# Optimization experiments

Hardware: AMD Instinct MI355X
Metric: run time of the kernel (lower is better)

Reference implementation:

```python
import jax, jax.numpy as jnp
import numpy as np

B, T, C = 4, 2048, 1024
H = 16
DH = C // H  # 64


def setup_inputs() -> dict:
    key = jax.random.key(0)
    ks = jax.random.split(key, 6)
    s = 1.0 / np.sqrt(C)
    x = jax.random.normal(ks[0], (B, T, C), dtype=jnp.float32)
    # per-head projection weights, stacked: (H, C, DH)
    Wq = jax.random.uniform(ks[1], (H, C, DH), dtype=jnp.float32, minval=-s, maxval=s)
    Wk = jax.random.uniform(ks[2], (H, C, DH), dtype=jnp.float32, minval=-s, maxval=s)
    Wv = jax.random.uniform(ks[3], (H, C, DH), dtype=jnp.float32, minval=-s, maxval=s)
    # output projection (torch Linear: y = x @ W.T + b); store as (C, C) for x @ Wo
    Wo = jax.random.uniform(ks[4], (C, C), dtype=jnp.float32, minval=-s, maxval=s)
    bo = jax.random.uniform(ks[5], (C,), dtype=jnp.float32, minval=-s, maxval=s)
    return {"x": x, "Wq": Wq, "Wk": Wk, "Wv": Wv, "Wo": Wo, "bo": bo}


def reference(x, Wq, Wk, Wv, Wo, bo):
    # x: (B,T,C) -> q,k,v: (B,H,T,DH)
    q = jnp.einsum('btc,hcd->bhtd', x, Wq)
    k = jnp.einsum('btc,hcd->bhtd', x, Wk)
    v = jnp.einsum('btc,hcd->bhtd', x, Wv)
    scale = DH ** -0.5
    scores = jnp.einsum('bhtd,bhsd->bhts', q, k) * scale  # (B,H,T,T)
    causal = jnp.tril(jnp.ones((T, T), dtype=bool))
    scores = jnp.where(causal, scores, -jnp.inf)
    wei = jax.nn.softmax(scores, axis=-1)
    out = jnp.einsum('bhts,bhsd->bhtd', wei, v)  # (B,H,T,DH)
    # concat heads: (B,T,H*DH) = (B,T,C)
    out = out.transpose(0, 2, 1, 3).reshape(B, T, C)
    return out @ Wo + bo
```

## Files before the change

kernel.cpp:

```cpp
#include <hip/hip_runtime.h>

#define T_SEQ 2048
#define C_DIM 1024
#define H_NUM 16
#define DHD   64
#define B_NUM 4
#define M_ROWS (B_NUM*T_SEQ)

typedef __bf16 bf16x8 __attribute__((ext_vector_type(8)));
typedef float  f32x4  __attribute__((ext_vector_type(4)));
typedef unsigned short ushort8 __attribute__((ext_vector_type(8)));
typedef unsigned short ushort4e __attribute__((ext_vector_type(4)));

__device__ __forceinline__ unsigned short f2b(float f){
  return __builtin_bit_cast(unsigned short, (__bf16)f);
}
__device__ __forceinline__ bf16x8 as_bf(ushort8 u){ return __builtin_bit_cast(bf16x8, u); }
__device__ __forceinline__ float exp2fast(float x){ return __builtin_amdgcn_exp2f(x); }

__device__ __forceinline__ void gload16(const void* g, void* l){
  __builtin_amdgcn_global_load_lds(
      (const __attribute__((address_space(1))) void*)g,
      (__attribute__((address_space(3))) void*)l, 16, 0, 0);
}

__global__ __launch_bounds__(256) void k_conv_x(const float* __restrict__ x,
                                                unsigned short* __restrict__ xb){
  int i = blockIdx.x*256 + threadIdx.x;
  float4 f = ((const float4*)x)[i];
  ushort4e o;
  o[0]=f2b(f.x); o[1]=f2b(f.y); o[2]=f2b(f.z); o[3]=f2b(f.w);
  ((ushort4e*)xb)[i] = o;
}

__global__ __launch_bounds__(256) void k_pack_w(const float* __restrict__ wq,
                                                const float* __restrict__ wk,
                                                const float* __restrict__ wv,
                                                const float* __restrict__ wo,
                                                unsigned short* __restrict__ wt,
                                                unsigned short* __restrict__ wot){
  int idx = blockIdx.x*256 + threadIdx.x;
  if (idx < 3*C_DIM*C_DIM){
    int nall = idx >> 10; int c = idx & 1023;
    int m = nall >> 10;   int n = nall & 1023;
    int h = n >> 6, d = n & 63;
    const float* w = (m==0) ? wq : (m==1) ? wk : wv;
    float f = w[((size_t)h*C_DIM + c)*DHD + d];
    if (m == 0) f *= 0.125f * 1.4426950408889634f;
    wt[idx] = f2b(f);
  } else {
    int j = idx - 3*C_DIM*C_DIM;
    int n = j >> 10, c = j & 1023;
    wot[j] = f2b(wo[(size_t)c*C_DIM + n]);
  }
}

__global__ __launch_bounds__(256) void k_gemm_qkv(const unsigned short* __restrict__ xb,
                                                  const unsigned short* __restrict__ wt,
                                                  unsigned short* __restrict__ qo,
                                                  unsigned short* __restrict__ ko,
                                                  unsigned short* __restrict__ vtr){
  __shared__ __align__(16) unsigned short smem[2][128*64];
  const int tid = threadIdx.x, lane = tid & 63, wid = tid >> 6;
  const int g = lane >> 4, tl = lane & 15;
  const int wr = wid >> 1, wc = wid & 1;
  const int id = blockIdx.x;
  const int swz = (id & 7)*192 + (id >> 3);
  const int mbase = (swz / 24) * 128, nbase = (swz % 24) * 128;
  f32x4 acc[4][4] = {};
  for (int kk = 0; kk < C_DIM; kk += 64){
    __syncthreads();
    #pragma unroll
    for (int i = 0; i < 4; i++){
      const int brow = (wid*4 + i)*8;
      const int row  = brow + (lane >> 3);
      const int jj   = (lane & 7) ^ (row & 7);
      gload16(&xb[(size_t)(mbase+row)*C_DIM + kk + jj*8], &smem[0][brow*64]);
      gload16(&wt[(size_t)(nbase+row)*C_DIM + kk + jj*8], &smem[1][brow*64]);
    }
    __syncthreads();
    bf16x8 aF[4][2], bF[4][2];
    #pragma unroll
    for (int mb = 0; mb < 4; mb++){
      const int row = wr*64 + mb*16 + tl; const int s7 = row & 7;
      aF[mb][0] = as_bf(*(const ushort8*)&smem[0][row*64 + ((g     ^ s7)*8)]);
      aF[mb][1] = as_bf(*(const ushort8*)&smem[0][row*64 + (((4+g) ^ s7)*8)]);
    }
    #pragma unroll
    for (int nb = 0; nb < 4; nb++){
      const int row = wc*64 + nb*16 + tl; const int s7 = row & 7;
      bF[nb][0] = as_bf(*(const ushort8*)&smem[1][row*64 + ((g     ^ s7)*8)]);
      bF[nb][1] = as_bf(*(const ushort8*)&smem[1][row*64 + (((4+g) ^ s7)*8)]);
    }
    #pragma unroll
    for (int mb = 0; mb < 4; mb++)
      #pragma unroll
      for (int nb = 0; nb < 4; nb++){
        acc[mb][nb] = __builtin_amdgcn_mfma_f32_16x16x32_bf16(aF[mb][0], bF[nb][0], acc[mb][nb], 0,0,0);
        acc[mb][nb] = __builtin_amdgcn_mfma_f32_16x16x32_bf16(aF[mb][1], bF[nb][1], acc[mb][nb], 0,0,0);
      }
  }
  const int sel = nbase >> 10;
  if (sel < 2){
    unsigned short* dst0 = (sel == 0) ? qo : ko;
    #pragma unroll
    for (int mb = 0; mb < 4; mb++){
      #pragma unroll
      for (int nb = 0; nb < 4; nb++){
        #pragma unroll
        for (int r = 0; r < 4; r++){
          int gr = mbase + wr*64 + mb*16 + g*4 + r;
          int gc = nbase + wc*64 + nb*16 + tl;
          int b = gr >> 11, t = gr & 2047;
          int nw = gc & 1023;
          int h = nw >> 6, d = nw & 63;
          dst0[(((size_t)(b*H_NUM + h))*T_SEQ + t)*DHD + d] = f2b(acc[mb][nb][r]);
        }
      }
    }
  } else {
    __syncthreads();
    unsigned short* tr = &smem[0][0];
    #pragma unroll
    for (int mb = 0; mb < 4; mb++){
      #pragma unroll
      for (int nb = 0; nb < 4; nb++){
        const int n = wc*64 + nb*16 + tl;
        const int m0 = wr*64 + mb*16 + g*4;
        ushort4e pk;
        #pragma unroll
        for (int r = 0; r < 4; r++) pk[r] = f2b(acc[mb][nb][r]);
        *(ushort4e*)&tr[n*128 + (m0 ^ ((n & 15) << 3))] = pk;
      }
    }
    __syncthreads();
    const int hbase = (nbase - 2048) >> 6;
    const int b = mbase >> 11, tloc = mbase & 2047;
    const int n = tid >> 1, half = tid & 1;
    unsigned short* vdst = vtr + (((size_t)(b*H_NUM + hbase + (n >> 6)))*DHD + (n & 63))*T_SEQ
                           + tloc + half*64;
    #pragma unroll
    for (int c8 = 0; c8 < 8; c8++){
      const int chunk = (half*8 + c8) ^ (n & 15);
      *(ushort8*)&vdst[c8*8] = *(const ushort8*)&tr[n*128 + chunk*8];
    }
  }
}

__global__ __launch_bounds__(512) void k_flash(const unsigned short* __restrict__ q,
                                               const unsigned short* __restrict__ k,
                                               const unsigned short* __restrict__ vtg,
                                               unsigned short* __restrict__ o){
  __shared__ __align__(16) unsigned short kbufs[2][64*64];
  __shared__ __align__(16) unsigned short vbufs[2][64*64];
  __shared__ __align__(16) unsigned short pl[8][32][72];
  const int tid = threadIdx.x, lane = tid & 63, w = tid >> 6;
  const int g = lane >> 4, tl = lane & 15;
  const int id = blockIdx.x;
  const int swz = (id & 7)*32 + (id >> 3);
  const int bh = swz >> 2, bx = swz & 3;
  const int b = bh >> 4, h = bh & 15;
  const unsigned short* qb = q   + (size_t)bh * T_SEQ * DHD;
  const unsigned short* kb = k   + (size_t)bh * T_SEQ * DHD;
  const unsigned short* vb = vtg + (size_t)bh * (size_t)DHD * T_SEQ;
  const int lrow = lane >> 3, lj = lane & 7;

  for (int pass = 0; pass < 2; ++pass){
    const int qt = pass ? (7 - bx) : bx;
    const int tbase = qt * 256;
    const int trow0 = tbase + w * 32;
    const int tmax = trow0 + 31;
    bf16x8 qF[2][2];
    #pragma unroll
    for (int tf = 0; tf < 2; tf++)
      #pragma unroll
      for (int ks = 0; ks < 2; ks++)
        qF[tf][ks] = as_bf(*(const ushort8*)&qb[(size_t)(trow0 + tf*16 + tl)*DHD + ks*32 + g*8]);
    f32x4 acc[2][4] = {};
    float mreg[2] = {-1e30f, -1e30f}, lreg[2] = {0.f, 0.f};
    const int nkt = 4*qt + 4;
    {
      const int row = w*8 + lrow;
      const int jj = lj ^ (row & 7);
      gload16(&kb[(size_t)row*DHD + jj*8],   &kbufs[0][w*8*64]);
      gload16(&vb[(size_t)row*T_SEQ + jj*8], &vbufs[0][w*8*64]);
    }
    __syncthreads();
    for (int kti = 0; kti < nkt; ++kti){
      const int cur = kti & 1;
      const int kbase = kti * 64;
      if (kti + 1 < nkt){
        const int kb2 = kbase + 64;
        const int row = w*8 + lrow;
        const int jj = lj ^ (row & 7);
        gload16(&kb[(size_t)(kb2+row)*DHD + jj*8],   &kbufs[cur^1][w*8*64]);
        gload16(&vb[(size_t)row*T_SEQ + kb2 + jj*8], &vbufs[cur^1][w*8*64]);
      }
      if (kbase <= tmax){
        const unsigned short* kcur = kbufs[cur];
        const unsigned short* vcur = vbufs[cur];
        const int s7 = tl & 7;
        f32x4 st[2][4] = {};
        __builtin_amdgcn_s_setprio(1);
        #pragma unroll
        for (int sf = 0; sf < 4; sf++){
          const int row = sf*16 + tl;
          bf16x8 kf0 = as_bf(*(const ushort8*)&kcur[row*64 + ((g     ^ s7)*8)]);
          bf16x8 kf1 = as_bf(*(const ushort8*)&kcur[row*64 + (((4+g) ^ s7)*8)]);
          #pragma unroll
          for (int tf = 0; tf < 2; tf++){
            st[tf][sf] = __builtin_amdgcn_mfma_f32_16x16x32_bf16(kf0, qF[tf][0], st[tf][sf], 0,0,0);
            st[tf][sf] = __builtin_amdgcn_mfma_f32_16x16x32_bf16(kf1, qF[tf][1], st[tf][sf], 0,0,0);
          }
        }
        __builtin_amdgcn_s_setprio(0);
        if (kbase + 63 > trow0){
          #pragma unroll
          for (int tf = 0; tf < 2; tf++){
            int tg = trow0 + tf*16 + tl;
            #pragma unroll
            for (int sf = 0; sf < 4; sf++)
              #pragma unroll
              for (int r = 0; r < 4; r++)
                if (kbase + sf*16 + g*4 + r > tg) st[tf][sf][r] = -1e30f;
          }
        }
        #pragma unroll
        for (int tf = 0; tf < 2; tf++){
          float mloc = -1e30f;
          #pragma unroll
          for (int sf = 0; sf < 4; sf++)
            #pragma unroll
            for (int r = 0; r < 4; r++) mloc = fmaxf(mloc, st[tf][sf][r]);
          if (__any(mloc > mreg[tf] + 8.f)){
            float mrow = fmaxf(mloc, __shfl_xor(mloc, 16));
            mrow = fmaxf(mrow, __shfl_xor(mrow, 32));
            float mnew = fmaxf(mreg[tf], mrow);
            float alpha = exp2fast(mreg[tf] - mnew);
            mreg[tf] = mnew;
            lreg[tf] *= alpha;
            #pragma unroll
            for (int df = 0; df < 4; df++)
              #pragma unroll
              for (int r = 0; r < 4; r++) acc[tf][df][r] *= alpha;
          }
          float sum = 0.f;
          #pragma unroll
          for (int sf = 0; sf < 4; sf++){
            ushort4e pk;
            #pragma unroll
            for (int r = 0; r < 4; r++){
              float p = exp2fast(st[tf][sf][r] - mreg[tf]);
              sum += p;
              pk[r] = f2b(p);
            }
            *(ushort4e*)&pl[w][tf*16 + tl][sf*16 + g*4] = pk;
          }
          lreg[tf] += sum;
        }
        bf16x8 pa[2][2];
        #pragma unroll
        for (int tf = 0; tf < 2; tf++)
          #pragma unroll
          for (int ks = 0; ks < 2; ks++)
            pa[tf][ks] = as_bf(*(const ushort8*)&pl[w][tf*16 + tl][ks*32 + g*8]);
        __builtin_amdgcn_s_setprio(1);
        #pragma unroll
        for (int df = 0; df < 4; df++){
          const int row = df*16 + tl;
          bf16x8 vf0 = as_bf(*(const ushort8*)&vcur[row*64 + ((g     ^ s7)*8)]);
          bf16x8 vf1 = as_bf(*(const ushort8*)&vcur[row*64 + (((4+g) ^ s7)*8)]);
          #pragma unroll
          for (int tf = 0; tf < 2; tf++){
            acc[tf][df] = __builtin_amdgcn_mfma_f32_16x16x32_bf16(vf0, pa[tf][0], acc[tf][df], 0,0,0);
            acc[tf][df] = __builtin_amdgcn_mfma_f32_16x16x32_bf16(vf1, pa[tf][1], acc[tf][df], 0,0,0);
          }
        }
        __builtin_amdgcn_s_setprio(0);
      }
      __syncthreads();
    }
    #pragma unroll
    for (int tf = 0; tf < 2; tf++){
      float l = lreg[tf];
      l += __shfl_xor(l, 16);
      l += __shfl_xor(l, 32);
      float inv = 1.f / l;
      int tg = trow0 + tf*16 + tl;
      #pragma unroll
      for (int df = 0; df < 4; df++){
        ushort4e ov;
        #pragma unroll
        for (int r = 0; r < 4; r++) ov[r] = f2b(acc[tf][df][r] * inv);
        *(ushort4e*)&o[((size_t)(b*T_SEQ + tg))*C_DIM + h*DHD + df*16 + g*4] = ov;
      }
    }
  }
}

__global__ __launch_bounds__(256) void k_gemm_proj(const unsigned short* __restrict__ ab,
                                                   const unsigned short* __restrict__ wot,
                                                   const float* __restrict__ bo,
                                                   float* __restrict__ out){
  __shared__ __align__(16) unsigned short a_lds[128*64];
  __shared__ __align__(16) unsigned short b_lds[128*64];
  const int tid = threadIdx.x, lane = tid & 63, wid = tid >> 6;
  const int g = lane >> 4, tl = lane & 15;
  const int wr = wid >> 1, wc = wid & 1;
  const int id = blockIdx.x;
  const int swz = (id & 7)*64 + (id >> 3);
  const int mbase = (swz >> 3) * 128, nbase = (swz & 7) * 128;
  f32x4 acc[4][4] = {};
  for (int kk = 0; kk < C_DIM; kk += 64){
    __syncthreads();
    #pragma unroll
    for (int i = 0; i < 4; i++){
      const int brow = (wid*4 + i)*8;
      const int row  = brow + (lane >> 3);
      const int jj   = (lane & 7) ^ (row & 7);
      gload16(&ab[(size_t)(mbase+row)*C_DIM + kk + jj*8],  &a_lds[brow*64]);
      gload16(&wot[(size_t)(nbase+row)*C_DIM + kk + jj*8], &b_lds[brow*64]);
    }
    __syncthreads();
    bf16x8 aF[4][2], bF[4][2];
    #pragma unroll
    for (int mb = 0; mb < 4; mb++){
      const int row = wr*64 + mb*16 + tl; const int s7 = row & 7;
      aF[mb][0] = as_bf(*(const ushort8*)&a_lds[row*64 + ((g     ^ s7)*8)]);
      aF[mb][1] = as_bf(*(const ushort8*)&a_lds[row*64 + (((4+g) ^ s7)*8)]);
    }
    #pragma unroll
    for (int nb = 0; nb < 4; nb++){
      const int row = wc*64 + nb*16 + tl; const int s7 = row & 7;
      bF[nb][0] = as_bf(*(const ushort8*)&b_lds[row*64 + ((g     ^ s7)*8)]);
      bF[nb][1] = as_bf(*(const ushort8*)&b_lds[row*64 + (((4+g) ^ s7)*8)]);
    }
    #pragma unroll
    for (int mb = 0; mb < 4; mb++)
      #pragma unroll
      for (int nb = 0; nb < 4; nb++){
        acc[mb][nb] = __builtin_amdgcn_mfma_f32_16x16x32_bf16(aF[mb][0], bF[nb][0], acc[mb][nb], 0,0,0);
        acc[mb][nb] = __builtin_amdgcn_mfma_f32_16x16x32_bf16(aF[mb][1], bF[nb][1], acc[mb][nb], 0,0,0);
      }
  }
  #pragma unroll
  for (int mb = 0; mb < 4; mb++){
    #pragma unroll
    for (int nb = 0; nb < 4; nb++){
      #pragma unroll
      for (int r = 0; r < 4; r++){
        int gr = mbase + wr*64 + mb*16 + g*4 + r;
        int gc = nbase + wc*64 + nb*16 + tl;
        out[(size_t)gr*C_DIM + gc] = acc[mb][nb][r] + bo[gc];
      }
    }
  }
}

extern "C" void kernel_launch(void* const* d_in, const int* in_sizes, int n_in,
                              void* d_out, int out_size, void* d_ws, size_t ws_size,
                              hipStream_t stream){
  const float* x  = (const float*)d_in[0];
  const float* Wq = (const float*)d_in[1];
  const float* Wk = (const float*)d_in[2];
  const float* Wv = (const float*)d_in[3];
  const float* Wo = (const float*)d_in[4];
  const float* bo = (const float*)d_in[5];
  float* out = (float*)d_out;

  char* p = (char*)d_ws;
  unsigned short* xb  = (unsigned short*)p; p += (size_t)M_ROWS*C_DIM*2;
  unsigned short* wt  = (unsigned short*)p; p += (size_t)3*C_DIM*C_DIM*2;
  unsigned short* wot = (unsigned short*)p; p += (size_t)C_DIM*C_DIM*2;
  unsigned short* Qb  = (unsigned short*)p; p += (size_t)M_ROWS*C_DIM*2;
  unsigned short* Kb  = (unsigned short*)p; p += (size_t)M_ROWS*C_DIM*2;
  unsigned short* Vtr = (unsigned short*)p; p += (size_t)M_ROWS*C_DIM*2;
  unsigned short* attn = xb;

  hipLaunchKernelGGL(k_conv_x, dim3(M_ROWS*C_DIM/4/256), dim3(256), 0, stream, x, xb);
  hipLaunchKernelGGL(k_pack_w, dim3(4*C_DIM*C_DIM/256), dim3(256), 0, stream,
                     Wq, Wk, Wv, Wo, wt, wot);
  hipLaunchKernelGGL(k_gemm_qkv, dim3(1536), dim3(256), 0, stream,
                     xb, wt, Qb, Kb, Vtr);
  hipLaunchKernelGGL(k_flash, dim3(256), dim3(512), 0, stream,
                     Qb, Kb, Vtr, attn);
  hipLaunchKernelGGL(k_gemm_proj, dim3(512), dim3(256), 0, stream,
                     attn, wot, bo, out);
}
```

Measured before the change: 183.3 us.

## Keep softmax probabilities in registers and merge prep kernels into one launch

The flash kernel no longer writes the exp'd scores to an LDS staging buffer and reads them back. It packs them straight into bf16 MFMA operands in registers, and reorders how V fragments are read from LDS so their k-index layout matches the accumulator layout. This removes the per-wave LDS round trip and the 36KB of shared memory it used, which may also allow higher occupancy. Separately, the x conversion and weight packing kernels are merged into one launch to save a kernel launch. The V loads are now two 8-byte reads per fragment instead of one 16-byte read.

```diff
diff --git a/kernel.cpp b/kernel.cpp
--- a/kernel.cpp
+++ b/kernel.cpp
@@ -24,34 +24,38 @@
       (__attribute__((address_space(3))) void*)l, 16, 0, 0);
 }
 
-__global__ __launch_bounds__(256) void k_conv_x(const float* __restrict__ x,
-                                                unsigned short* __restrict__ xb){
-  int i = blockIdx.x*256 + threadIdx.x;
-  float4 f = ((const float4*)x)[i];
-  ushort4e o;
-  o[0]=f2b(f.x); o[1]=f2b(f.y); o[2]=f2b(f.z); o[3]=f2b(f.w);
-  ((ushort4e*)xb)[i] = o;
-}
-
-__global__ __launch_bounds__(256) void k_pack_w(const float* __restrict__ wq,
-                                                const float* __restrict__ wk,
-                                                const float* __restrict__ wv,
-                                                const float* __restrict__ wo,
-                                                unsigned short* __restrict__ wt,
-                                                unsigned short* __restrict__ wot){
-  int idx = blockIdx.x*256 + threadIdx.x;
-  if (idx < 3*C_DIM*C_DIM){
-    int nall = idx >> 10; int c = idx & 1023;
-    int m = nall >> 10;   int n = nall & 1023;
-    int h = n >> 6, d = n & 63;
-    const float* w = (m==0) ? wq : (m==1) ? wk : wv;
-    float f = w[((size_t)h*C_DIM + c)*DHD + d];
-    if (m == 0) f *= 0.125f * 1.4426950408889634f;
-    wt[idx] = f2b(f);
+#define MF(a,b,c) __builtin_amdgcn_mfma_f32_16x16x32_bf16(a,b,c,0,0,0)
+
+__global__ __launch_bounds__(256) void k_prep(const float* __restrict__ x,
+                                              const float* __restrict__ wq,
+                                              const float* __restrict__ wk,
+                                              const float* __restrict__ wv,
+                                              const float* __restrict__ wo,
+                                              unsigned short* __restrict__ xb,
+                                              unsigned short* __restrict__ wt,
+                                              unsigned short* __restrict__ wot){
+  const int bid = blockIdx.x;
+  if (bid < 8192){
+    int i = bid*256 + threadIdx.x;
+    float4 f = ((const float4*)x)[i];
+    ushort4e o;
+    o[0]=f2b(f.x); o[1]=f2b(f.y); o[2]=f2b(f.z); o[3]=f2b(f.w);
+    ((ushort4e*)xb)[i] = o;
   } else {
-    int j = idx - 3*C_DIM*C_DIM;
-    int n = j >> 10, c = j & 1023;
-    wot[j] = f2b(wo[(size_t)c*C_DIM + n]);
+    int idx = (bid - 8192)*256 + threadIdx.x;
+    if (idx < 3*C_DIM*C_DIM){
+      int nall = idx >> 10; int c = idx & 1023;
+      int m = nall >> 10;   int n = nall & 1023;
+      int h = n >> 6, d = n & 63;
+      const float* w = (m==0) ? wq : (m==1) ? wk : wv;
+      float f = w[((size_t)h*C_DIM + c)*DHD + d];
+      if (m == 0) f *= 0.125f * 1.4426950408889634f;
+      wt[idx] = f2b(f);
+    } else {
+      int j = idx - 3*C_DIM*C_DIM;
+      int n = j >> 10, c = j & 1023;
+      wot[j] = f2b(wo[(size_t)c*C_DIM + n]);
+    }
   }
 }
 
@@ -96,8 +100,8 @@
     for (int mb = 0; mb < 4; mb++)
       #pragma unroll
       for (int nb = 0; nb < 4; nb++){
-        acc[mb][nb] = __builtin_amdgcn_mfma_f32_16x16x32_bf16(aF[mb][0], bF[nb][0], acc[mb][nb], 0,0,0);
-        acc[mb][nb] = __builtin_amdgcn_mfma_f32_16x16x32_bf16(aF[mb][1], bF[nb][1], acc[mb][nb], 0,0,0);
+        acc[mb][nb] = MF(aF[mb][0], bF[nb][0], acc[mb][nb]);
+        acc[mb][nb] = MF(aF[mb][1], bF[nb][1], acc[mb][nb]);
       }
   }
   const int sel = nbase >> 10;
@@ -153,7 +157,6 @@
                                                unsigned short* __restrict__ o){
   __shared__ __align__(16) unsigned short kbufs[2][64*64];
   __shared__ __align__(16) unsigned short vbufs[2][64*64];
-  __shared__ __align__(16) unsigned short pl[8][32][72];
   const int tid = threadIdx.x, lane = tid & 63, w = tid >> 6;
   const int g = lane >> 4, tl = lane & 15;
   const int id = blockIdx.x;
@@ -209,8 +212,8 @@
           bf16x8 kf1 = as_bf(*(const ushort8*)&kcur[row*64 + (((4+g) ^ s7)*8)]);
           #pragma unroll
           for (int tf = 0; tf < 2; tf++){
-            st[tf][sf] = __builtin_amdgcn_mfma_f32_16x16x32_bf16(kf0, qF[tf][0], st[tf][sf], 0,0,0);
-            st[tf][sf] = __builtin_amdgcn_mfma_f32_16x16x32_bf16(kf1, qF[tf][1], st[tf][sf], 0,0,0);
+            st[tf][sf] = MF(kf0, qF[tf][0], st[tf][sf]);
+            st[tf][sf] = MF(kf1, qF[tf][1], st[tf][sf]);
           }
         }
         __builtin_amdgcn_s_setprio(0);
@@ -246,34 +249,46 @@
           }
           float sum = 0.f;
           #pragma unroll
-          for (int sf = 0; sf < 4; sf++){
-            ushort4e pk;
+          for (int sf = 0; sf < 4; sf++)
             #pragma unroll
             for (int r = 0; r < 4; r++){
               float p = exp2fast(st[tf][sf][r] - mreg[tf]);
               sum += p;
-              pk[r] = f2b(p);
+              st[tf][sf][r] = p;
             }
-            *(ushort4e*)&pl[w][tf*16 + tl][sf*16 + g*4] = pk;
-          }
           lreg[tf] += sum;
         }
         bf16x8 pa[2][2];
         #pragma unroll
         for (int tf = 0; tf < 2; tf++)
           #pragma unroll
-          for (int ks = 0; ks < 2; ks++)
-            pa[tf][ks] = as_bf(*(const ushort8*)&pl[w][tf*16 + tl][ks*32 + g*8]);
+          for (int ks = 0; ks < 2; ks++){
+            ushort8 u;
+            #pragma unroll
+            for (int r = 0; r < 4; r++){
+              u[r]   = f2b(st[tf][2*ks  ][r]);
+              u[4+r] = f2b(st[tf][2*ks+1][r]);
+            }
+            pa[tf][ks] = as_bf(u);
+          }
         __builtin_amdgcn_s_setprio(1);
         #pragma unroll
         for (int df = 0; df < 4; df++){
           const int row = df*16 + tl;
-          bf16x8 vf0 = as_bf(*(const ushort8*)&vcur[row*64 + ((g     ^ s7)*8)]);
-          bf16x8 vf1 = as_bf(*(const ushort8*)&vcur[row*64 + (((4+g) ^ s7)*8)]);
+          bf16x8 vfr[2];
+          #pragma unroll
+          for (int ks = 0; ks < 2; ks++){
+            ushort4e lo = *(const ushort4e*)&vcur[row*64 + (((4*ks +     (g>>1)) ^ s7)*8) + 4*(g&1)];
+            ushort4e hi = *(const ushort4e*)&vcur[row*64 + (((4*ks + 2 + (g>>1)) ^ s7)*8) + 4*(g&1)];
+            ushort8 u;
+            #pragma unroll
+            for (int e = 0; e < 4; e++){ u[e] = lo[e]; u[4+e] = hi[e]; }
+            vfr[ks] = as_bf(u);
+          }
           #pragma unroll
           for (int tf = 0; tf < 2; tf++){
-            acc[tf][df] = __builtin_amdgcn_mfma_f32_16x16x32_bf16(vf0, pa[tf][0], acc[tf][df], 0,0,0);
-            acc[tf][df] = __builtin_amdgcn_mfma_f32_16x16x32_bf16(vf1, pa[tf][1], acc[tf][df], 0,0,0);
+            acc[tf][df] = MF(vfr[0], pa[tf][0], acc[tf][df]);
+            acc[tf][df] = MF(vfr[1], pa[tf][1], acc[tf][df]);
           }
         }
         __builtin_amdgcn_s_setprio(0);
@@ -339,8 +354,8 @@
     for (int mb = 0; mb < 4; mb++)
       #pragma unroll
       for (int nb = 0; nb < 4; nb++){
-        acc[mb][nb] = __builtin_amdgcn_mfma_f32_16x16x32_bf16(aF[mb][0], bF[nb][0], acc[mb][nb], 0,0,0);
-        acc[mb][nb] = __builtin_amdgcn_mfma_f32_16x16x32_bf16(aF[mb][1], bF[nb][1], acc[mb][nb], 0,0,0);
+        acc[mb][nb] = MF(aF[mb][0], bF[nb][0], acc[mb][nb]);
+        acc[mb][nb] = MF(aF[mb][1], bF[nb][1], acc[mb][nb]);
       }
   }
   #pragma unroll
@@ -377,9 +392,8 @@
   unsigned short* Vtr = (unsigned short*)p; p += (size_t)M_ROWS*C_DIM*2;
   unsigned short* attn = xb;
 
-  hipLaunchKernelGGL(k_conv_x, dim3(M_ROWS*C_DIM/4/256), dim3(256), 0, stream, x, xb);
-  hipLaunchKernelGGL(k_pack_w, dim3(4*C_DIM*C_DIM/256), dim3(256), 0, stream,
-                     Wq, Wk, Wv, Wo, wt, wot);
+  hipLaunchKernelGGL(k_prep, dim3(8192 + 16384), dim3(256), 0, stream,
+                     x, Wq, Wk, Wv, Wo, xb, wt, wot);
   hipLaunchKernelGGL(k_gemm_qkv, dim3(1536), dim3(256), 0, stream,
                      xb, wt, Qb, Kb, Vtr);
   hipLaunchKernelGGL(k_flash, dim3(256), dim3(512), 0, stream,
```

Result: no change. 181.2 us (-1.1%).
